# Performance work log

Measured on AMD Instinct MI355X. Metric: run time of the kernel, lower is better.

## Reference

```python
import jax, jax.numpy as jnp
import numpy as np

KLD_BINS = 10
RATIO_KLD = 0.5
# categorical one-hot blocks in the 99-dim Adult encoding
BLOCKS = [(1, 8), (8, 24), (24, 31), (31, 45), (45, 51), (51, 53), (53, 55), (58, 99)]
CONT_COLS = np.array([0, 55, 56, 57])


def _cross_entropy(logits, onehot):
    # F.cross_entropy with targets = argmax of the one-hot block (mean over batch)
    logp = jax.nn.log_softmax(logits, axis=-1)
    return -jnp.mean(jnp.sum(onehot * logp, axis=-1))


def _kl_divergence(p, q):
    # np-style KL: sum p*log(p/q) over valid (nonzero) bins
    valid = (p > 0) & (q > 0)
    ratio = jnp.where(valid, p / jnp.where(valid, q, 1.0), 1.0)
    return jnp.sum(jnp.where(valid, p * jnp.log(ratio), 0.0))


def setup_inputs() -> dict:
    B = 262144
    key = jax.random.key(0)
    ks = jax.random.split(key, 16)
    data_decoded = jax.random.normal(ks[0], (B, 99), dtype=jnp.float32)
    # data_true: continuous columns + one-hot categorical blocks
    data_true = jnp.zeros((B, 99), dtype=jnp.float32)
    data_true = data_true.at[:, CONT_COLS].set(jax.random.normal(ks[1], (B, 4), dtype=jnp.float32))
    for j, (s, e) in enumerate(BLOCKS):
        lab = jax.random.randint(ks[2 + j], (B,), 0, e - s)
        data_true = data_true.at[:, s:e].set(jax.nn.one_hot(lab, e - s, dtype=jnp.float32))
    data_encoded = jax.random.normal(ks[11], (B, 12), dtype=jnp.float32)
    sex = jax.random.bernoulli(ks[12], 0.5, (B,)).astype(jnp.float32)
    data_encoded = data_encoded.at[:, 11].set(sex)  # column 11 of combined is the 0/1 sex neuron
    label_true = jax.random.normal(ks[13], (B, 2), dtype=jnp.float32)
    return {
        'data_encoded': data_encoded,
        'data_decoded': data_decoded,
        'data_true': data_true,
        'label_true': label_true,
        'batch_size': B,
    }


def reference(data_encoded, data_decoded, data_true, label_true, batch_size):
    # --- reconstruction MSE on continuous columns ---
    cc = jnp.asarray(CONT_COLS)
    mse_loss = jnp.sum(jnp.mean((data_decoded[:, cc] - data_true[:, cc]) ** 2, axis=0))
    # --- cross-entropy on each categorical block ---
    ce_loss = jnp.float32(0.0)
    for s, e in BLOCKS:
        ce_loss = ce_loss + _cross_entropy(data_decoded[:, s:e], data_true[:, s:e])
    # --- per-feature histogram KLD between male/female groups (no grad, as in torch via .numpy()) ---
    comb = jnp.concatenate([data_encoded, label_true], axis=1)  # [B, 14]
    feats = comb[:, :KLD_BINS]  # first 10 encoded features, [B, 10]
    mn = jnp.min(feats, axis=0)  # per-column min over full batch (torch .item())
    mx = jnp.max(feats, axis=0)
    width = jnp.maximum(mx - mn, 1e-12)
    # torch.histc bin index: floor((x-min)/(max-min)*bins), x==max -> last bin
    idx = jnp.clip(jnp.floor((feats - mn) / width * KLD_BINS).astype(jnp.int32), 0, KLD_BINS - 1)
    onehot = jax.nn.one_hot(idx, KLD_BINS, dtype=jnp.float32)  # [B, 10, bins]
    sexcol = comb[:, 11]
    m_mask = (sexcol == 0).astype(jnp.float32)
    f_mask = (sexcol == 1).astype(jnp.float32)
    m_count = jnp.maximum(jnp.sum(m_mask), 1.0)
    f_count = jnp.maximum(jnp.sum(f_mask), 1.0)
    m_hist = jnp.einsum('b,bik->ik', m_mask, onehot) / m_count  # [10, bins]
    f_hist = jnp.einsum('b,bik->ik', f_mask, onehot) / f_count
    kld = jax.lax.stop_gradient(_kl_divergence(m_hist, f_hist))
    alpha = RATIO_KLD
    multi_loss = (1.0 - alpha) * (mse_loss + ce_loss) + alpha * kld
    return (multi_loss, mse_loss, ce_loss, alpha * kld)
```

## Files before the change

kernel.cpp:

```cpp
#include <hip/hip_runtime.h>
#include <math.h>

#define B_ROWS 262144

#define WS_A 0
#define WS_B 2816
#define WS_C 28416
#define MAIN_BLOCKS 1536
#define N_WAVES (MAIN_BLOCKS * 4)
#define TILE_ROWS 8
#define N_TILES 32768
#define TILE_F4 198

__device__ __forceinline__ unsigned int map_f(float x) {
  unsigned int b = __float_as_uint(x);
  return (b & 0x80000000u) ? ~b : (b | 0x80000000u);
}
__device__ __forceinline__ float unmap_f(unsigned int u) {
  unsigned int b = (u & 0x80000000u) ? (u ^ 0x80000000u) : ~u;
  return __uint_as_float(b);
}

__global__ __launch_bounds__(256) void k_minmax(const float* __restrict__ enc,
                                                unsigned int* __restrict__ ws) {
  int tid = threadIdx.x, bid = blockIdx.x;
  const float4* e4 = (const float4*)enc;
  float mn[10], mx[10];
  #pragma unroll
  for (int j = 0; j < 10; j++) { mn[j] = 1e30f; mx[j] = -1e30f; }
  unsigned int cm = 0, cf = 0;
  #pragma unroll
  for (int i = 0; i < 8; i++) {
    size_t g = (size_t)bid * 2048 + i * 256 + tid;
    float4 a = e4[g * 3 + 0], b = e4[g * 3 + 1], c = e4[g * 3 + 2];
    float v[12] = {a.x,a.y,a.z,a.w,b.x,b.y,b.z,b.w,c.x,c.y,c.z,c.w};
    #pragma unroll
    for (int j = 0; j < 10; j++) { mn[j] = fminf(mn[j], v[j]); mx[j] = fmaxf(mx[j], v[j]); }
    cm += (v[11] == 0.0f); cf += (v[11] == 1.0f);
  }
  #pragma unroll
  for (int off = 32; off; off >>= 1) {
    #pragma unroll
    for (int j = 0; j < 10; j++) {
      mn[j] = fminf(mn[j], __shfl_xor(mn[j], off));
      mx[j] = fmaxf(mx[j], __shfl_xor(mx[j], off));
    }
    cm += __shfl_xor(cm, off); cf += __shfl_xor(cf, off);
  }
  __shared__ float smn[4][10], smx[4][10];
  __shared__ unsigned int sc[4][2];
  int wave = tid >> 6, lane = tid & 63;
  if (lane == 0) {
    #pragma unroll
    for (int j = 0; j < 10; j++) { smn[wave][j] = mn[j]; smx[wave][j] = mx[j]; }
    sc[wave][0] = cm; sc[wave][1] = cf;
  }
  __syncthreads();
  unsigned int* out = ws + WS_A + bid * 22;
  if (tid < 10) {
    float m = fminf(fminf(smn[0][tid], smn[1][tid]), fminf(smn[2][tid], smn[3][tid]));
    out[tid] = map_f(m);
  } else if (tid < 20) {
    int j = tid - 10;
    float m = fmaxf(fmaxf(smx[0][j], smx[1][j]), fmaxf(smx[2][j], smx[3][j]));
    out[tid] = map_f(m);
  } else if (tid < 22) {
    int j = tid - 20;
    out[tid] = sc[0][j] + sc[1][j] + sc[2][j] + sc[3][j];
  }
}

__global__ __launch_bounds__(256) void k_hist(const float* __restrict__ enc,
                                              unsigned int* __restrict__ ws) {
  __shared__ float mnv[10], wid[10];
  __shared__ unsigned int h[200];
  int tid = threadIdx.x, bid = blockIdx.x;
  for (int i = tid; i < 200; i += 256) h[i] = 0u;
  if (tid < 10) {
    unsigned int umn = 0xFFFFFFFFu, umx = 0u;
    #pragma unroll 4
    for (int b = 0; b < 128; b++) {
      umn = min(umn, ws[WS_A + b * 22 + tid]);
      umx = max(umx, ws[WS_A + b * 22 + 10 + tid]);
    }
    float mn = unmap_f(umn);
    mnv[tid] = mn;
    wid[tid] = fmaxf(unmap_f(umx) - mn, 1e-12f);
  }
  __syncthreads();
  const float4* e4 = (const float4*)enc;
  #pragma unroll
  for (int i = 0; i < 8; i++) {
    size_t g = (size_t)bid * 2048 + i * 256 + tid;
    float4 a = e4[g * 3 + 0], b = e4[g * 3 + 1], c = e4[g * 3 + 2];
    float v[12] = {a.x,a.y,a.z,a.w,b.x,b.y,b.z,b.w,c.x,c.y,c.z,c.w};
    int base = (v[11] == 0.0f) ? 0 : ((v[11] == 1.0f) ? 100 : -1);
    if (base >= 0) {
      #pragma unroll
      for (int cc = 0; cc < 10; cc++) {
        float t = (v[cc] - mnv[cc]) / wid[cc] * 10.0f;
        int bi = min(max((int)floorf(t), 0), 9);
        atomicAdd(&h[base + cc * 10 + bi], 1u);
      }
    }
  }
  __syncthreads();
  if (tid < 200) ws[WS_B + bid * 200 + tid] = h[tid];
}

__global__ __launch_bounds__(256, 6) void k_main(const float* __restrict__ d,
                                                 const float* __restrict__ t,
                                                 unsigned int* __restrict__ ws) {
  __shared__ float sd[4][800];
  __shared__ float red[12];
  int tid = threadIdx.x, bid = blockIdx.x;
  int wave = tid >> 6, lane = tid & 63;
  float* ldsd = sd[wave];
  float4* lw4 = (float4*)ldsd;
  int gw = bid * 4 + wave;

  float mse = 0.f, dot = 0.f, ce = 0.f;

  for (int tile = gw; tile < N_TILES; tile += N_WAVES) {
    const float4* ds = (const float4*)d + (size_t)tile * TILE_F4;
    const float4* ts = (const float4*)t + (size_t)tile * TILE_F4;
    int cl = (lane < 6) ? lane : 0;
    float4 d0 = ds[lane],       t0 = ts[lane];
    float4 d1 = ds[64 + lane],  t1 = ts[64 + lane];
    float4 d2 = ds[128 + lane], t2 = ts[128 + lane];
    float4 d3 = ds[192 + cl],   t3 = ts[192 + cl];
    float4 dv4[4] = {d0, d1, d2, d3};
    float4 tv4[4] = {t0, t1, t2, t3};
    #pragma unroll
    for (int it = 0; it < 4; ++it) {
      if (it < 3 || lane < 6) {
        int f = it * 64 + lane;
        float4 xd = dv4[it];
        float4 xt = tv4[it];
        int e = f * 4;
        int c = e - (e / 99) * 99;
        float dv[4] = {xd.x, xd.y, xd.z, xd.w};
        float tw[4] = {xt.x, xt.y, xt.z, xt.w};
        #pragma unroll
        for (int k = 0; k < 4; k++) {
          int cc = c + k;
          if (cc >= 99) cc -= 99;
          bool cont = (cc == 0) | ((unsigned)(cc - 55) <= 2u);
          float diff = dv[k] - tw[k];
          if (cont) mse += diff * diff;
          else      dot += tw[k] * dv[k];
        }
        float4 ev;
        ev.x = __expf(xd.x); ev.y = __expf(xd.y);
        ev.z = __expf(xd.z); ev.w = __expf(xd.w);
        lw4[f] = ev;
      }
    }
    if (lane < 2 * TILE_ROWS) {
      const float* row = ldsd + (lane >> 1) * 99;
      float Z;
      if ((lane & 1) == 0) {
        Z = 0.f;
        #pragma unroll
        for (int c = 1; c < 8; c++) Z += row[c];
        ce += __logf(Z);
        Z = 0.f;
        #pragma unroll
        for (int c = 8; c < 24; c++) Z += row[c];
        ce += __logf(Z);
        Z = 0.f;
        #pragma unroll
        for (int c = 24; c < 31; c++) Z += row[c];
        ce += __logf(Z);
        Z = 0.f;
        #pragma unroll
        for (int c = 31; c < 45; c++) Z += row[c];
        ce += __logf(Z);
        Z = 0.f;
        #pragma unroll
        for (int c = 45; c < 51; c++) Z += row[c];
        ce += __logf(Z);
      } else {
        Z = 0.f;
        #pragma unroll
        for (int c = 51; c < 53; c++) Z += row[c];
        ce += __logf(Z);
        Z = 0.f;
        #pragma unroll
        for (int c = 53; c < 55; c++) Z += row[c];
        ce += __logf(Z);
        float Za = 0.f, Zb = 0.f;
        #pragma unroll
        for (int c = 58; c < 78; c++) Za += row[c];
        #pragma unroll
        for (int c = 78; c < 99; c++) Zb += row[c];
        ce += __logf(Za + Zb);
      }
    }
  }

  #pragma unroll
  for (int off = 32; off; off >>= 1) {
    mse += __shfl_xor(mse, off);
    dot += __shfl_xor(dot, off);
    ce  += __shfl_xor(ce,  off);
  }
  if (lane == 0) { red[wave] = mse; red[4 + wave] = dot; red[8 + wave] = ce; }
  __syncthreads();
  if (tid == 0) {
    float* C = (float*)(ws + WS_C);
    C[bid]                   = red[0] + red[1] + red[2]  + red[3];
    C[MAIN_BLOCKS + bid]     = red[4] + red[5] + red[6]  + red[7];
    C[2 * MAIN_BLOCKS + bid] = red[8] + red[9] + red[10] + red[11];
  }
}

__global__ __launch_bounds__(256) void k_final(const unsigned int* __restrict__ ws,
                                               float* __restrict__ out) {
  __shared__ float h[200];
  __shared__ float part[256];
  __shared__ float red3[12];
  __shared__ float cnts[2];
  int tid = threadIdx.x;
  if (tid < 200) {
    unsigned int s = 0;
    #pragma unroll 4
    for (int b = 0; b < 128; b++) s += ws[WS_B + b * 200 + tid];
    h[tid] = (float)s;
  }
  if (tid == 200 || tid == 201) {
    unsigned int s = 0;
    #pragma unroll 4
    for (int b = 0; b < 128; b++) s += ws[WS_A + b * 22 + 20 + (tid - 200)];
    cnts[tid - 200] = fmaxf((float)s, 1.0f);
  }
  const float* C = (const float*)(ws + WS_C);
  float msum = 0.f, dsum = 0.f, csum = 0.f;
  for (int i = tid; i < MAIN_BLOCKS; i += 256) {
    msum += C[i]; dsum += C[MAIN_BLOCKS + i]; csum += C[2 * MAIN_BLOCKS + i];
  }
  #pragma unroll
  for (int off = 32; off; off >>= 1) {
    msum += __shfl_xor(msum, off);
    dsum += __shfl_xor(dsum, off);
    csum += __shfl_xor(csum, off);
  }
  int wave = tid >> 6, lane = tid & 63;
  if (lane == 0) { red3[wave] = msum; red3[4 + wave] = dsum; red3[8 + wave] = csum; }
  __syncthreads();
  float term = 0.f;
  if (tid < 100) {
    float mc = h[tid], fc = h[100 + tid];
    if (mc > 0.f && fc > 0.f) {
      float p = mc / cnts[0];
      float q = fc / cnts[1];
      term = p * logf(p / q);
    }
  }
  part[tid] = term;
  __syncthreads();
  for (int s = 128; s; s >>= 1) {
    if (tid < s) part[tid] += part[tid + s];
    __syncthreads();
  }
  if (tid == 0) {
    const float invB = 1.0f / (float)B_ROWS;
    float mse = (red3[0] + red3[1] + red3[2] + red3[3]) * invB;
    float dd  = (red3[4] + red3[5] + red3[6] + red3[7]);
    float cc  = (red3[8] + red3[9] + red3[10] + red3[11]);
    float ce  = (cc - dd) * invB;
    float akld = 0.5f * part[0];
    out[0] = 0.5f * (mse + ce) + akld;
    out[1] = mse;
    out[2] = ce;
    out[3] = akld;
  }
}

extern "C" void kernel_launch(void* const* d_in, const int* in_sizes, int n_in,
                              void* d_out, int out_size, void* d_ws, size_t ws_size,
                              hipStream_t stream) {
  const float* enc = (const float*)d_in[0];
  const float* dec = (const float*)d_in[1];
  const float* tru = (const float*)d_in[2];
  unsigned int* ws = (unsigned int*)d_ws;
  float* out = (float*)d_out;

  hipLaunchKernelGGL(k_minmax, dim3(128),         dim3(256), 0, stream, enc, ws);
  hipLaunchKernelGGL(k_hist,   dim3(128),         dim3(256), 0, stream, enc, ws);
  hipLaunchKernelGGL(k_main,   dim3(MAIN_BLOCKS), dim3(256), 0, stream, dec, tru, ws);
  hipLaunchKernelGGL(k_final,  dim3(1),           dim3(256), 0, stream, ws, out);
}
```

Measured before the change: 266.8 us.

## Double-buffer decoded tiles via async global-to-LDS loads with prefetch

Loads of the decoded tensor now go straight from global memory into LDS using global_load_lds, into a per-wave double buffer. The next tile is prefetched while the current one is processed, and manual s_waitcnt plus sched_barrier control when the data is ready. The aim is to hide global load latency in this memory-bound reduction. It doubles LDS use per block, which may reduce occupancy, and relies on fragile hand-written waitcnt counts such as vmcnt(8) that must match the number of loads issued.

```diff
diff --git a/kernel.cpp b/kernel.cpp
--- a/kernel.cpp
+++ b/kernel.cpp
@@ -108,34 +108,55 @@
   if (tid < 200) ws[WS_B + bid * 200 + tid] = h[tid];
 }
 
+__device__ __forceinline__ void issue_d(const float* __restrict__ d,
+                                        int tile, int lane, float* bd) {
+  const float4* dsp = (const float4*)d + (size_t)tile * TILE_F4;
+  #pragma unroll
+  for (int it = 0; it < 3; ++it)
+    __builtin_amdgcn_global_load_lds(
+        (const __attribute__((address_space(1))) void*)(dsp + it * 64 + lane),
+        (__attribute__((address_space(3))) void*)(bd + it * 256), 16, 0, 0);
+  if (lane < 6)
+    __builtin_amdgcn_global_load_lds(
+        (const __attribute__((address_space(1))) void*)(dsp + 192 + lane),
+        (__attribute__((address_space(3))) void*)(bd + 768), 16, 0, 0);
+}
+
 __global__ __launch_bounds__(256, 6) void k_main(const float* __restrict__ d,
                                                  const float* __restrict__ t,
                                                  unsigned int* __restrict__ ws) {
-  __shared__ float sd[4][800];
+  __shared__ float sd[4][2][800];
   __shared__ float red[12];
   int tid = threadIdx.x, bid = blockIdx.x;
   int wave = tid >> 6, lane = tid & 63;
-  float* ldsd = sd[wave];
-  float4* lw4 = (float4*)ldsd;
+  float* base = &sd[wave][0][0];
   int gw = bid * 4 + wave;
 
   float mse = 0.f, dot = 0.f, ce = 0.f;
-
+  int cl = (lane < 6) ? lane : 0;
+
+  int p = 0;
+  issue_d(d, gw, lane, base);
   for (int tile = gw; tile < N_TILES; tile += N_WAVES) {
-    const float4* ds = (const float4*)d + (size_t)tile * TILE_F4;
+    int nx = tile + N_WAVES;
+    int pf = (nx < N_TILES) ? nx : tile;
     const float4* ts = (const float4*)t + (size_t)tile * TILE_F4;
-    int cl = (lane < 6) ? lane : 0;
-    float4 d0 = ds[lane],       t0 = ts[lane];
-    float4 d1 = ds[64 + lane],  t1 = ts[64 + lane];
-    float4 d2 = ds[128 + lane], t2 = ts[128 + lane];
-    float4 d3 = ds[192 + cl],   t3 = ts[192 + cl];
-    float4 dv4[4] = {d0, d1, d2, d3};
+    float4 t0 = ts[lane];
+    float4 t1 = ts[64 + lane];
+    float4 t2 = ts[128 + lane];
+    float4 t3 = ts[192 + cl];
+    asm volatile("s_waitcnt lgkmcnt(0)" ::: "memory");
+    issue_d(d, pf, lane, base + (p ^ 1) * 800);
+    asm volatile("s_waitcnt vmcnt(8)" ::: "memory");
+    __builtin_amdgcn_sched_barrier(0);
+    float* ldsd = base + p * 800;
+    float4* lb4 = (float4*)ldsd;
     float4 tv4[4] = {t0, t1, t2, t3};
     #pragma unroll
     for (int it = 0; it < 4; ++it) {
       if (it < 3 || lane < 6) {
         int f = it * 64 + lane;
-        float4 xd = dv4[it];
+        float4 xd = lb4[f];
         float4 xt = tv4[it];
         int e = f * 4;
         int c = e - (e / 99) * 99;
@@ -153,9 +174,11 @@
         float4 ev;
         ev.x = __expf(xd.x); ev.y = __expf(xd.y);
         ev.z = __expf(xd.z); ev.w = __expf(xd.w);
-        lw4[f] = ev;
+        lb4[f] = ev;
       }
     }
+    asm volatile("s_waitcnt lgkmcnt(0)" ::: "memory");
+    __builtin_amdgcn_sched_barrier(0);
     if (lane < 2 * TILE_ROWS) {
       const float* row = ldsd + (lane >> 1) * 99;
       float Z;
@@ -197,7 +220,9 @@
         ce += __logf(Za + Zb);
       }
     }
-  }
+    p ^= 1;
+  }
+  asm volatile("s_waitcnt vmcnt(0)" ::: "memory");
 
   #pragma unroll
   for (int off = 32; off; off >>= 1) {
```

Result: no change. 268.2 us (+0.5%).
